# Performance work log

Hardware: AMD Instinct MI355X
Metric: run time of the kernel (lower is better)

The kernel has to match this reference:

```python
import jax, jax.numpy as jnp
import numpy as np

HEADS = 16
DIM_HEAD = 64
NPATCH = 256
LN_EPS = 1e-5


def setup_inputs() -> dict:
    key = jax.random.key(0)
    ks = jax.random.split(key, 6)
    B, S, D = 4, 2048, 1024
    inner = HEADS * DIM_HEAD  # 1024
    x = jax.random.normal(ks[0], (B, S, D), dtype=jnp.float32)
    ln_gamma = jnp.ones((D,), dtype=jnp.float32)
    ln_beta = jnp.zeros((D,), dtype=jnp.float32)
    # torch Linear: y = x @ W.T; we store the transposed weight directly.
    Wqkv = jax.random.normal(ks[1], (D, 3 * inner), dtype=jnp.float32) / np.sqrt(D)
    Wout = jax.random.normal(ks[2], (inner, D), dtype=jnp.float32) / np.sqrt(inner)
    bout = jnp.zeros((D,), dtype=jnp.float32)
    return {"x": x, "ln_gamma": ln_gamma, "ln_beta": ln_beta,
            "Wqkv": Wqkv, "Wout": Wout, "bout": bout}


def reference(x, ln_gamma, ln_beta, Wqkv, Wout, bout):
    B, S, D = x.shape
    # LayerNorm
    mu = jnp.mean(x, axis=-1, keepdims=True)
    var = jnp.mean(jnp.square(x - mu), axis=-1, keepdims=True)
    xn = (x - mu) * jax.lax.rsqrt(var + LN_EPS) * ln_gamma + ln_beta
    # QKV projection
    qkv = xn @ Wqkv  # [B, S, 3*H*Dh]
    q, k, v = jnp.split(qkv, 3, axis=-1)
    q = q.reshape(B, S, HEADS, DIM_HEAD)
    k = k.reshape(B, S, HEADS, DIM_HEAD)
    v = v.reshape(B, S, HEADS, DIM_HEAD)
    scale = DIM_HEAD ** -0.5
    dots = jnp.einsum('bqhd,bkhd->bhqk', q, k) * scale  # [B,H,S,S]
    # block-causal mask: query window i attends to key windows 0..i
    win = jnp.arange(S) // NPATCH
    mask = win[:, None] >= win[None, :]  # [S, S] bool
    dots = jnp.where(mask[None, None], dots, -jnp.inf)
    attn = jax.nn.softmax(dots, axis=-1)
    out = jnp.einsum('bhqk,bkhd->bqhd', attn, v).reshape(B, S, HEADS * DIM_HEAD)
    return out @ Wout + bout
```

## Files before the change

kernel.cpp:

```cpp
#include <hip/hip_runtime.h>
#include <stdint.h>

typedef unsigned short u16;
typedef __attribute__((ext_vector_type(8))) short bf16x8;
typedef __attribute__((ext_vector_type(4))) float f32x4;
typedef __attribute__((ext_vector_type(4))) unsigned short u16x4;
typedef __attribute__((ext_vector_type(4))) unsigned int u32x4;

#define DEVI static __device__ __forceinline__

#define QSCALE (0.125f * 1.4426950408889634f)

DEVI u16 f2bf(float f) {
  union { float f; unsigned int u; } v; v.f = f;
  unsigned int u = v.u + 0x7fffu + ((v.u >> 16) & 1u);
  return (u16)(u >> 16);
}
DEVI void gl16(const void* g, void* l) {
  __builtin_amdgcn_global_load_lds(
      (__attribute__((address_space(1))) void*)g,
      (__attribute__((address_space(3))) void*)l, 16, 0, 0);
}
DEVI unsigned int cvtpk(float a, float b) {
  unsigned int r;
  asm("v_cvt_pk_bf16_f32 %0, %1, %2" : "=v"(r) : "v"(a), "v"(b));
  return r;
}

__device__ const int QTMAP[16] = {15, 14, 13, 12, 8, 9, 10, 11,
                                  5, 4, 6, 7, 2, 3, 1, 0};

__global__ __launch_bounds__(256) void k_ln_split(
    const float* __restrict__ x, const float* __restrict__ gamma,
    const float* __restrict__ beta, u16* __restrict__ xh) {
  const int row = blockIdx.x;
  const int t = threadIdx.x;
  const float4* xr = (const float4*)(x + (size_t)row * 1024);
  float4 v = xr[t];
  float s = v.x + v.y + v.z + v.w;
  float s2 = v.x * v.x + v.y * v.y + v.z * v.z + v.w * v.w;
  #pragma unroll
  for (int m = 1; m < 64; m <<= 1) { s += __shfl_xor(s, m); s2 += __shfl_xor(s2, m); }
  __shared__ float ls[4], ls2[4];
  if ((t & 63) == 0) { ls[t >> 6] = s; ls2[t >> 6] = s2; }
  __syncthreads();
  s = ls[0] + ls[1] + ls[2] + ls[3];
  s2 = ls2[0] + ls2[1] + ls2[2] + ls2[3];
  float mu = s * (1.0f / 1024.0f);
  float var = s2 * (1.0f / 1024.0f) - mu * mu;
  float rstd = rsqrtf(var + 1e-5f);
  float4 g = ((const float4*)gamma)[t];
  float4 b = ((const float4*)beta)[t];
  float xv[4] = {v.x, v.y, v.z, v.w};
  float gg[4] = {g.x, g.y, g.z, g.w};
  float bb[4] = {b.x, b.y, b.z, b.w};
  u16x4 hv;
  #pragma unroll
  for (int i = 0; i < 4; i++) {
    float xn = (xv[i] - mu) * rstd * gg[i] + bb[i];
    hv[i] = f2bf(xn);
  }
  ((u16x4*)xh)[(size_t)row * 256 + t] = hv;
}

__global__ __launch_bounds__(256) void k_wsplit_t(
    const float* __restrict__ W, u16* __restrict__ Wth, int K, int N) {
  __shared__ float tile[32][33];
  const int t = threadIdx.x;
  const int tx = t & 31, ty = t >> 5;
  #pragma unroll
  for (int i = 0; i < 4; i++) {
    int k = blockIdx.y * 32 + ty + i * 8;
    int n = blockIdx.x * 32 + tx;
    tile[ty + i * 8][tx] = W[(size_t)k * N + n];
  }
  __syncthreads();
  #pragma unroll
  for (int i = 0; i < 4; i++) {
    int n = blockIdx.x * 32 + ty + i * 8;
    int k = blockIdx.y * 32 + tx;
    Wth[(size_t)n * K + k] = f2bf(tile[tx][ty + i * 8]);
  }
}

template <int MODE>
__global__ __launch_bounds__(256) void k_gemm(
    const u16* __restrict__ Ah, const u16* __restrict__ Bh,
    u16* __restrict__ Qh, u16* __restrict__ Kh, u16* __restrict__ Vth,
    float* __restrict__ Cout, const float* __restrict__ bias) {
  __shared__ u16 sAh[128 * 64];
  __shared__ u16 sBh[128 * 64];
  const int t = threadIdx.x, lane = t & 63, w = t >> 6;
  const int bm = blockIdx.x, bn = blockIdx.y;
  const int wm = (w >> 1) * 64, wn = (w & 1) * 64;
  const int g = lane >> 4, c = lane & 15;
  const size_t arow0 = (size_t)bm * 128, brow0 = (size_t)bn * 128;

  f32x4 acc[4][4] = {};

  for (int kt = 0; kt < 16; kt++) {
    __syncthreads();
    #pragma unroll
    for (int i = 0; i < 4; i++) {
      int ci = t + i * 256;
      int r = ci >> 3, cc = ci & 7;
      int cs = cc ^ (r & 7);
      size_t ka = (size_t)kt * 64 + cs * 8;
      gl16(Ah + (arow0 + r) * 1024 + ka, sAh + (size_t)ci * 8);
      gl16(Bh + (brow0 + r) * 1024 + ka, sBh + (size_t)ci * 8);
    }
    __syncthreads();
    #pragma unroll
    for (int ks = 0; ks < 2; ks++) {
      bf16x8 afh[4], bfh[4];
      #pragma unroll
      for (int mi = 0; mi < 4; mi++) {
        int row = wm + mi * 16 + c;
        afh[mi] = *(const bf16x8*)(sAh + row * 64 + (((ks * 4 + g) ^ (row & 7)) * 8));
      }
      #pragma unroll
      for (int ni = 0; ni < 4; ni++) {
        int row = wn + ni * 16 + c;
        bfh[ni] = *(const bf16x8*)(sBh + row * 64 + (((ks * 4 + g) ^ (row & 7)) * 8));
      }
      #pragma unroll
      for (int mi = 0; mi < 4; mi++)
        #pragma unroll
        for (int ni = 0; ni < 4; ni++)
          acc[mi][ni] = __builtin_amdgcn_mfma_f32_16x16x32_bf16(afh[mi], bfh[ni], acc[mi][ni], 0, 0, 0);
    }
  }

  if (MODE == 0) {
    #pragma unroll
    for (int mi = 0; mi < 4; mi++) {
      int grow0 = bm * 128 + wm + mi * 16 + g * 4;
      int b = grow0 >> 11, s0 = grow0 & 2047;
      #pragma unroll
      for (int ni = 0; ni < 4; ni++) {
        int gcol = bn * 128 + wn + ni * 16 + c;
        int which = gcol >> 10, rem = gcol & 1023;
        int hh = rem >> 6, dd = rem & 63;
        if (which == 2) {
          u16x4 hv;
          #pragma unroll
          for (int r = 0; r < 4; r++) hv[r] = f2bf(acc[mi][ni][r]);
          size_t off = ((size_t)((b * 16 + hh) * 64 + dd)) * 2048 + s0;
          *(u16x4*)(Vth + off) = hv;
        } else {
          u16* dh = which ? Kh : Qh;
          float sc = which ? 1.0f : QSCALE;
          #pragma unroll
          for (int r = 0; r < 4; r++) {
            size_t off = ((size_t)(b * 16 + hh) * 2048 + (s0 + r)) * 64 + dd;
            dh[off] = f2bf(acc[mi][ni][r] * sc);
          }
        }
      }
    }
  } else {
    #pragma unroll
    for (int mi = 0; mi < 4; mi++) {
      int grow0 = bm * 128 + wm + mi * 16 + g * 4;
      #pragma unroll
      for (int ni = 0; ni < 4; ni++) {
        int gcol = bn * 128 + wn + ni * 16 + c;
        float bb = bias[gcol];
        #pragma unroll
        for (int r = 0; r < 4; r++)
          Cout[(size_t)(grow0 + r) * 1024 + gcol] = acc[mi][ni][r] + bb;
      }
    }
  }
}

__global__ __launch_bounds__(512, 4) void k_attn(
    const u16* __restrict__ Qh, const u16* __restrict__ Kh,
    const u16* __restrict__ Vth, u16* __restrict__ Oh) {
  __shared__ u16 lK[2][64 * 64], lV[2][64 * 64];
  const int t = threadIdx.x, lane = t & 63, w = t >> 6;
  const int bh = blockIdx.x;
  const int qt = QTMAP[blockIdx.y];
  const int b = bh >> 4, h = bh & 15;
  const int qrow0 = qt * 128;
  const int kvlen = (qt / 2 + 1) * 256;
  const int g = lane >> 4, c = lane & 15;

  bf16x8 qf[2];
  {
    const u16* qb = Qh + ((size_t)bh * 2048 + qrow0 + w * 16) * 64;
    #pragma unroll
    for (int ks = 0; ks < 2; ks++)
      qf[ks] = *(const bf16x8*)(qb + (size_t)c * 64 + ks * 32 + g * 8);
  }

  const u16* Kb = Kh + (size_t)bh * 2048 * 64;
  const u16* Vb = Vth + (size_t)bh * 64 * 2048;

  const int ci = t;
  const int r0 = ci >> 3, cc0 = ci & 7;
  const int cs0 = cc0 ^ (r0 & 7);

  float mrun = -INFINITY, lrun = 0.f;
  f32x4 o[4] = {};

  const int ntiles = kvlen >> 6;

  gl16(Kb + (size_t)r0 * 64 + cs0 * 8, lK[0] + (size_t)ci * 8);
  gl16(Vb + (size_t)r0 * 2048 + cs0 * 8, lV[0] + (size_t)ci * 8);
  __syncthreads();

  const u16* gK = Kb + (size_t)(64 + r0) * 64 + cs0 * 8;
  const u16* gV = Vb + (size_t)r0 * 2048 + 64 + cs0 * 8;

  for (int kt = 0; kt < ntiles; kt++) {
    const int cur = kt & 1, nxt = cur ^ 1;
    if (kt + 1 < ntiles) {
      gl16(gK, lK[nxt] + (size_t)ci * 8);  gK += 64 * 64;
      gl16(gV, lV[nxt] + (size_t)ci * 8);  gV += 64;
    }

    f32x4 s[4] = {};
    __builtin_amdgcn_s_setprio(1);
    #pragma unroll
    for (int ni = 0; ni < 4; ni++) {
      int kr = ni * 16 + c;
      #pragma unroll
      for (int ks = 0; ks < 2; ks++) {
        int off = kr * 64 + ((ks * 4 + g) ^ (kr & 7)) * 8;
        bf16x8 kf = *(const bf16x8*)(lK[cur] + off);
        s[ni] = __builtin_amdgcn_mfma_f32_16x16x32_bf16(kf, qf[ks], s[ni], 0, 0, 0);
      }
    }
    __builtin_amdgcn_s_setprio(0);

    float a0 = fmaxf(fmaxf(s[0][0], s[0][1]), fmaxf(s[0][2], s[0][3]));
    float a1 = fmaxf(fmaxf(s[1][0], s[1][1]), fmaxf(s[1][2], s[1][3]));
    float a2 = fmaxf(fmaxf(s[2][0], s[2][1]), fmaxf(s[2][2], s[2][3]));
    float a3 = fmaxf(fmaxf(s[3][0], s[3][1]), fmaxf(s[3][2], s[3][3]));
    float tl = fmaxf(fmaxf(a0, a1), fmaxf(a2, a3));
    if (!__all(tl - mrun <= 8.0f)) {
      float tm = tl;
      tm = fmaxf(tm, __shfl_xor(tm, 16));
      tm = fmaxf(tm, __shfl_xor(tm, 32));
      float mnew = fmaxf(mrun, tm);
      float al = exp2f(mrun - mnew);
      mrun = mnew;
      lrun *= al;
      #pragma unroll
      for (int r = 0; r < 4; r++) {
        float ar = __shfl(al, g * 4 + r);
        #pragma unroll
        for (int di = 0; di < 4; di++) o[di][r] *= ar;
      }
    }

    #pragma unroll
    for (int ni = 0; ni < 4; ni++)
      #pragma unroll
      for (int r = 0; r < 4; r++)
        s[ni][r] = exp2f(s[ni][r] - mrun);
    #pragma unroll
    for (int ni = 0; ni < 4; ni++)
      lrun += (s[ni][0] + s[ni][1]) + (s[ni][2] + s[ni][3]);
    unsigned int Wd[4][2];
    #pragma unroll
    for (int ni = 0; ni < 4; ni++)
      #pragma unroll
      for (int rp = 0; rp < 2; rp++)
        Wd[ni][rp] = cvtpk(s[ni][2 * rp], s[ni][2 * rp + 1]);
    bf16x8 pa[2];
    #pragma unroll
    for (int ks = 0; ks < 2; ks++) {
      unsigned int e0 = Wd[2 * ks][0], f0 = Wd[2 * ks + 1][0];
      unsigned int e1 = Wd[2 * ks][1], f1 = Wd[2 * ks + 1][1];
      asm volatile("v_permlane32_swap_b32 %0, %1" : "+v"(e0), "+v"(f0));
      asm volatile("v_permlane16_swap_b32 %0, %1" : "+v"(e0), "+v"(f0));
      asm volatile("v_permlane32_swap_b32 %0, %1" : "+v"(e1), "+v"(f1));
      asm volatile("v_permlane16_swap_b32 %0, %1" : "+v"(e1), "+v"(f1));
      union { u32x4 u; bf16x8 bv; } cvu;
      cvu.u = (u32x4){e0, e1, f0, f1};
      pa[ks] = cvu.bv;
    }

    __builtin_amdgcn_s_setprio(1);
    #pragma unroll
    for (int di = 0; di < 4; di++) {
      int vr = di * 16 + c;
      #pragma unroll
      for (int ks = 0; ks < 2; ks++) {
        int off = vr * 64 + ((ks * 4 + g) ^ (vr & 7)) * 8;
        bf16x8 vf = *(const bf16x8*)(lV[cur] + off);
        o[di] = __builtin_amdgcn_mfma_f32_16x16x32_bf16(pa[ks], vf, o[di], 0, 0, 0);
      }
    }
    __builtin_amdgcn_s_setprio(0);

    __syncthreads();
  }

  float lf = lrun;
  lf += __shfl_xor(lf, 16);
  lf += __shfl_xor(lf, 32);
  float inv = 1.0f / lf;
  #pragma unroll
  for (int r = 0; r < 4; r++) {
    float ir = __shfl(inv, g * 4 + r);
    int srow = qrow0 + w * 16 + g * 4 + r;
    size_t rowo = ((size_t)b * 2048 + srow) * 1024 + h * 64;
    #pragma unroll
    for (int di = 0; di < 4; di++)
      Oh[rowo + di * 16 + c] = f2bf(o[di][r] * ir);
  }
}

extern "C" void kernel_launch(void* const* d_in, const int* in_sizes, int n_in,
                              void* d_out, int out_size, void* d_ws, size_t ws_size,
                              hipStream_t stream) {
  const float* x     = (const float*)d_in[0];
  const float* gamma = (const float*)d_in[1];
  const float* beta  = (const float*)d_in[2];
  const float* Wqkv  = (const float*)d_in[3];
  const float* Wout  = (const float*)d_in[4];
  const float* bout  = (const float*)d_in[5];
  float* out = (float*)d_out;

  char* ws = (char*)d_ws;
  size_t off = 0;
  auto alloc = [&](size_t bytes) { char* p = ws + off; off += (bytes + 255) & ~(size_t)255; return p; };
  const size_t SZ_XN = (size_t)8192 * 1024 * 2;
  const size_t SZ_WQ = (size_t)3072 * 1024 * 2;
  const size_t SZ_WO = (size_t)1024 * 1024 * 2;
  const size_t SZ_QKV = (size_t)4 * 16 * 2048 * 64 * 2;
  u16* xnh  = (u16*)alloc(SZ_XN);
  u16* wqth = (u16*)alloc(SZ_WQ);
  u16* woth = (u16*)alloc(SZ_WO);
  u16* Qh  = (u16*)alloc(SZ_QKV);
  u16* Kh  = (u16*)alloc(SZ_QKV);
  u16* Vth = (u16*)alloc(SZ_QKV);
  if (off > ws_size) return;

  k_ln_split<<<8192, 256, 0, stream>>>(x, gamma, beta, xnh);
  k_wsplit_t<<<dim3(96, 32), 256, 0, stream>>>(Wqkv, wqth, 1024, 3072);
  k_wsplit_t<<<dim3(32, 32), 256, 0, stream>>>(Wout, woth, 1024, 1024);
  k_gemm<0><<<dim3(64, 24), 256, 0, stream>>>(xnh, wqth,
                                              Qh, Kh, Vth, nullptr, nullptr);
  k_attn<<<dim3(64, 16), 512, 0, stream>>>(Qh, Kh, Vth, xnh);
  k_gemm<1><<<dim3(64, 8), 256, 0, stream>>>(xnh, woth,
                                             nullptr, nullptr, nullptr,
                                             out, bout);
}
```

Before: 180.2 us.

## Pair heavy and light query tiles per attention block and swizzle GEMM tile order

The attention kernel now runs two query tiles per block, pairing tile 15-y with tile y, so every block does an equal amount of block-causal work and the grid is halved; this replaces the static QTMAP ordering. LDS read offsets for the K/V fragments are precomputed once per thread, and the row-max reduction is regrouped. The GEMM kernels remap block indices with an 8-way XCD-style swizzle so that neighbouring tiles share L2. The halved attention grid reduces parallelism (512 blocks), and the second tile reloads K/V from scratch.

```diff
diff --git a/kernel.cpp b/kernel.cpp
--- a/kernel.cpp
+++ b/kernel.cpp
@@ -26,9 +26,6 @@
   asm("v_cvt_pk_bf16_f32 %0, %1, %2" : "=v"(r) : "v"(a), "v"(b));
   return r;
 }
-
-__device__ const int QTMAP[16] = {15, 14, 13, 12, 8, 9, 10, 11,
-                                  5, 4, 6, 7, 2, 3, 1, 0};
 
 __global__ __launch_bounds__(256) void k_ln_split(
     const float* __restrict__ x, const float* __restrict__ gamma,
@@ -91,7 +88,10 @@
   __shared__ u16 sAh[128 * 64];
   __shared__ u16 sBh[128 * 64];
   const int t = threadIdx.x, lane = t & 63, w = t >> 6;
-  const int bm = blockIdx.x, bn = blockIdx.y;
+  const int flat = blockIdx.y * gridDim.x + blockIdx.x;
+  const int per = (gridDim.x * gridDim.y) >> 3;
+  const int swz = (flat & 7) * per + (flat >> 3);
+  const int bm = swz & 63, bn = swz >> 6;
   const int wm = (w >> 1) * 64, wn = (w & 1) * 64;
   const int g = lane >> 4, c = lane & 15;
   const size_t arow0 = (size_t)bm * 128, brow0 = (size_t)bn * 128;
@@ -180,137 +180,143 @@
   __shared__ u16 lK[2][64 * 64], lV[2][64 * 64];
   const int t = threadIdx.x, lane = t & 63, w = t >> 6;
   const int bh = blockIdx.x;
-  const int qt = QTMAP[blockIdx.y];
   const int b = bh >> 4, h = bh & 15;
-  const int qrow0 = qt * 128;
-  const int kvlen = (qt / 2 + 1) * 256;
   const int g = lane >> 4, c = lane & 15;
-
-  bf16x8 qf[2];
-  {
-    const u16* qb = Qh + ((size_t)bh * 2048 + qrow0 + w * 16) * 64;
-    #pragma unroll
-    for (int ks = 0; ks < 2; ks++)
-      qf[ks] = *(const bf16x8*)(qb + (size_t)c * 64 + ks * 32 + g * 8);
-  }
 
   const u16* Kb = Kh + (size_t)bh * 2048 * 64;
   const u16* Vb = Vth + (size_t)bh * 64 * 2048;
+
+  int roff[4][2];
+  #pragma unroll
+  for (int i = 0; i < 4; i++)
+    #pragma unroll
+    for (int ks = 0; ks < 2; ks++) {
+      int row = i * 16 + c;
+      roff[i][ks] = row * 64 + (((ks * 4 + g) ^ (row & 7)) * 8);
+    }
 
   const int ci = t;
   const int r0 = ci >> 3, cc0 = ci & 7;
   const int cs0 = cc0 ^ (r0 & 7);
 
-  float mrun = -INFINITY, lrun = 0.f;
-  f32x4 o[4] = {};
-
-  const int ntiles = kvlen >> 6;
-
-  gl16(Kb + (size_t)r0 * 64 + cs0 * 8, lK[0] + (size_t)ci * 8);
-  gl16(Vb + (size_t)r0 * 2048 + cs0 * 8, lV[0] + (size_t)ci * 8);
-  __syncthreads();
-
-  const u16* gK = Kb + (size_t)(64 + r0) * 64 + cs0 * 8;
-  const u16* gV = Vb + (size_t)r0 * 2048 + 64 + cs0 * 8;
-
-  for (int kt = 0; kt < ntiles; kt++) {
-    const int cur = kt & 1, nxt = cur ^ 1;
-    if (kt + 1 < ntiles) {
-      gl16(gK, lK[nxt] + (size_t)ci * 8);  gK += 64 * 64;
-      gl16(gV, lV[nxt] + (size_t)ci * 8);  gV += 64;
-    }
-
-    f32x4 s[4] = {};
-    __builtin_amdgcn_s_setprio(1);
-    #pragma unroll
-    for (int ni = 0; ni < 4; ni++) {
-      int kr = ni * 16 + c;
+  for (int half = 0; half < 2; half++) {
+    const int qt = half ? blockIdx.y : 15 - blockIdx.y;
+    const int qrow0 = qt * 128;
+    const int ntiles = ((qt >> 1) + 1) * 4;
+
+    bf16x8 qf[2];
+    {
+      const u16* qb = Qh + ((size_t)bh * 2048 + qrow0 + w * 16) * 64;
+      #pragma unroll
+      for (int ks = 0; ks < 2; ks++)
+        qf[ks] = *(const bf16x8*)(qb + (size_t)c * 64 + ks * 32 + g * 8);
+    }
+
+    float mrun = -INFINITY, lrun = 0.f;
+    f32x4 o[4] = {};
+
+    gl16(Kb + (size_t)r0 * 64 + cs0 * 8, lK[0] + (size_t)ci * 8);
+    gl16(Vb + (size_t)r0 * 2048 + cs0 * 8, lV[0] + (size_t)ci * 8);
+    __syncthreads();
+
+    const u16* gK = Kb + (size_t)(64 + r0) * 64 + cs0 * 8;
+    const u16* gV = Vb + (size_t)r0 * 2048 + 64 + cs0 * 8;
+
+    for (int kt = 0; kt < ntiles; kt++) {
+      const int cur = kt & 1, nxt = cur ^ 1;
+      if (kt + 1 < ntiles) {
+        gl16(gK, lK[nxt] + (size_t)ci * 8);  gK += 64 * 64;
+        gl16(gV, lV[nxt] + (size_t)ci * 8);  gV += 64;
+      }
+
+      f32x4 s[4] = {};
+      __builtin_amdgcn_s_setprio(1);
+      #pragma unroll
+      for (int ni = 0; ni < 4; ni++)
+        #pragma unroll
+        for (int ks = 0; ks < 2; ks++) {
+          bf16x8 kf = *(const bf16x8*)(lK[cur] + roff[ni][ks]);
+          s[ni] = __builtin_amdgcn_mfma_f32_16x16x32_bf16(kf, qf[ks], s[ni], 0, 0, 0);
+        }
+      __builtin_amdgcn_s_setprio(0);
+
+      float A0 = fmaxf(fmaxf(s[0][0], s[0][1]), s[0][2]);
+      float A1 = fmaxf(fmaxf(s[0][3], s[1][0]), s[1][1]);
+      float A2 = fmaxf(fmaxf(s[1][2], s[1][3]), s[2][0]);
+      float A3 = fmaxf(fmaxf(s[2][1], s[2][2]), s[2][3]);
+      float A4 = fmaxf(fmaxf(s[3][0], s[3][1]), s[3][2]);
+      float B0 = fmaxf(fmaxf(A0, A1), A2);
+      float tl = fmaxf(fmaxf(fmaxf(B0, A3), A4), s[3][3]);
+      if (!__all(tl - mrun <= 8.0f)) {
+        float tm = tl;
+        tm = fmaxf(tm, __shfl_xor(tm, 16));
+        tm = fmaxf(tm, __shfl_xor(tm, 32));
+        float mnew = fmaxf(mrun, tm);
+        float al = exp2f(mrun - mnew);
+        mrun = mnew;
+        lrun *= al;
+        #pragma unroll
+        for (int r = 0; r < 4; r++) {
+          float ar = __shfl(al, g * 4 + r);
+          #pragma unroll
+          for (int di = 0; di < 4; di++) o[di][r] *= ar;
+        }
+      }
+
+      #pragma unroll
+      for (int ni = 0; ni < 4; ni++)
+        #pragma unroll
+        for (int r = 0; r < 4; r++)
+          s[ni][r] = exp2f(s[ni][r] - mrun);
+      #pragma unroll
+      for (int ni = 0; ni < 4; ni++)
+        lrun += (s[ni][0] + s[ni][1]) + (s[ni][2] + s[ni][3]);
+      unsigned int Wd[4][2];
+      #pragma unroll
+      for (int ni = 0; ni < 4; ni++)
+        #pragma unroll
+        for (int rp = 0; rp < 2; rp++)
+          Wd[ni][rp] = cvtpk(s[ni][2 * rp], s[ni][2 * rp + 1]);
+      bf16x8 pa[2];
       #pragma unroll
       for (int ks = 0; ks < 2; ks++) {
-        int off = kr * 64 + ((ks * 4 + g) ^ (kr & 7)) * 8;
-        bf16x8 kf = *(const bf16x8*)(lK[cur] + off);
-        s[ni] = __builtin_amdgcn_mfma_f32_16x16x32_bf16(kf, qf[ks], s[ni], 0, 0, 0);
-      }
-    }
-    __builtin_amdgcn_s_setprio(0);
-
-    float a0 = fmaxf(fmaxf(s[0][0], s[0][1]), fmaxf(s[0][2], s[0][3]));
-    float a1 = fmaxf(fmaxf(s[1][0], s[1][1]), fmaxf(s[1][2], s[1][3]));
-    float a2 = fmaxf(fmaxf(s[2][0], s[2][1]), fmaxf(s[2][2], s[2][3]));
-    float a3 = fmaxf(fmaxf(s[3][0], s[3][1]), fmaxf(s[3][2], s[3][3]));
-    float tl = fmaxf(fmaxf(a0, a1), fmaxf(a2, a3));
-    if (!__all(tl - mrun <= 8.0f)) {
-      float tm = tl;
-      tm = fmaxf(tm, __shfl_xor(tm, 16));
-      tm = fmaxf(tm, __shfl_xor(tm, 32));
-      float mnew = fmaxf(mrun, tm);
-      float al = exp2f(mrun - mnew);
-      mrun = mnew;
-      lrun *= al;
-      #pragma unroll
-      for (int r = 0; r < 4; r++) {
-        float ar = __shfl(al, g * 4 + r);
-        #pragma unroll
-        for (int di = 0; di < 4; di++) o[di][r] *= ar;
-      }
-    }
-
-    #pragma unroll
-    for (int ni = 0; ni < 4; ni++)
-      #pragma unroll
-      for (int r = 0; r < 4; r++)
-        s[ni][r] = exp2f(s[ni][r] - mrun);
-    #pragma unroll
-    for (int ni = 0; ni < 4; ni++)
-      lrun += (s[ni][0] + s[ni][1]) + (s[ni][2] + s[ni][3]);
-    unsigned int Wd[4][2];
-    #pragma unroll
-    for (int ni = 0; ni < 4; ni++)
-      #pragma unroll
-      for (int rp = 0; rp < 2; rp++)
-        Wd[ni][rp] = cvtpk(s[ni][2 * rp], s[ni][2 * rp + 1]);
-    bf16x8 pa[2];
-    #pragma unroll
-    for (int ks = 0; ks < 2; ks++) {
-      unsigned int e0 = Wd[2 * ks][0], f0 = Wd[2 * ks + 1][0];
-      unsigned int e1 = Wd[2 * ks][1], f1 = Wd[2 * ks + 1][1];
-      asm volatile("v_permlane32_swap_b32 %0, %1" : "+v"(e0), "+v"(f0));
-      asm volatile("v_permlane16_swap_b32 %0, %1" : "+v"(e0), "+v"(f0));
-      asm volatile("v_permlane32_swap_b32 %0, %1" : "+v"(e1), "+v"(f1));
-      asm volatile("v_permlane16_swap_b32 %0, %1" : "+v"(e1), "+v"(f1));
-      union { u32x4 u; bf16x8 bv; } cvu;
-      cvu.u = (u32x4){e0, e1, f0, f1};
-      pa[ks] = cvu.bv;
-    }
-
-    __builtin_amdgcn_s_setprio(1);
-    #pragma unroll
-    for (int di = 0; di < 4; di++) {
-      int vr = di * 16 + c;
-      #pragma unroll
-      for (int ks = 0; ks < 2; ks++) {
-        int off = vr * 64 + ((ks * 4 + g) ^ (vr & 7)) * 8;
-        bf16x8 vf = *(const bf16x8*)(lV[cur] + off);
-        o[di] = __builtin_amdgcn_mfma_f32_16x16x32_bf16(pa[ks], vf, o[di], 0, 0, 0);
-      }
-    }
-    __builtin_amdgcn_s_setprio(0);
-
-    __syncthreads();
-  }
-
-  float lf = lrun;
-  lf += __shfl_xor(lf, 16);
-  lf += __shfl_xor(lf, 32);
-  float inv = 1.0f / lf;
-  #pragma unroll
-  for (int r = 0; r < 4; r++) {
-    float ir = __shfl(inv, g * 4 + r);
-    int srow = qrow0 + w * 16 + g * 4 + r;
-    size_t rowo = ((size_t)b * 2048 + srow) * 1024 + h * 64;
-    #pragma unroll
-    for (int di = 0; di < 4; di++)
-      Oh[rowo + di * 16 + c] = f2bf(o[di][r] * ir);
+        unsigned int e0 = Wd[2 * ks][0], f0 = Wd[2 * ks + 1][0];
+        unsigned int e1 = Wd[2 * ks][1], f1 = Wd[2 * ks + 1][1];
+        asm volatile("v_permlane32_swap_b32 %0, %1" : "+v"(e0), "+v"(f0));
+        asm volatile("v_permlane16_swap_b32 %0, %1" : "+v"(e0), "+v"(f0));
+        asm volatile("v_permlane32_swap_b32 %0, %1" : "+v"(e1), "+v"(f1));
+        asm volatile("v_permlane16_swap_b32 %0, %1" : "+v"(e1), "+v"(f1));
+        union { u32x4 u; bf16x8 bv; } cvu;
+        cvu.u = (u32x4){e0, e1, f0, f1};
+        pa[ks] = cvu.bv;
+      }
+
+      __builtin_amdgcn_s_setprio(1);
+      #pragma unroll
+      for (int di = 0; di < 4; di++)
+        #pragma unroll
+        for (int ks = 0; ks < 2; ks++) {
+          bf16x8 vf = *(const bf16x8*)(lV[cur] + roff[di][ks]);
+          o[di] = __builtin_amdgcn_mfma_f32_16x16x32_bf16(pa[ks], vf, o[di], 0, 0, 0);
+        }
+      __builtin_amdgcn_s_setprio(0);
+
+      __syncthreads();
+    }
+
+    float lf = lrun;
+    lf += __shfl_xor(lf, 16);
+    lf += __shfl_xor(lf, 32);
+    float inv = 1.0f / lf;
+    #pragma unroll
+    for (int r = 0; r < 4; r++) {
+      float ir = __shfl(inv, g * 4 + r);
+      int srow = qrow0 + w * 16 + g * 4 + r;
+      size_t rowo = ((size_t)b * 2048 + srow) * 1024 + h * 64;
+      #pragma unroll
+      for (int di = 0; di < 4; di++)
+        Oh[rowo + di * 16 + c] = f2bf(o[di][r] * ir);
+    }
   }
 }
 
@@ -345,7 +351,7 @@
   k_wsplit_t<<<dim3(32, 32), 256, 0, stream>>>(Wout, woth, 1024, 1024);
   k_gemm<0><<<dim3(64, 24), 256, 0, stream>>>(xnh, wqth,
                                               Qh, Kh, Vth, nullptr, nullptr);
-  k_attn<<<dim3(64, 16), 512, 0, stream>>>(Qh, Kh, Vth, xnh);
+  k_attn<<<dim3(64, 8), 512, 0, stream>>>(Qh, Kh, Vth, xnh);
   k_gemm<1><<<dim3(64, 8), 256, 0, stream>>>(xnh, woth,
                                              nullptr, nullptr, nullptr,
                                              out, bout);
```

Result: slower. 196.3 us (+9.0%).

## Widen attention KV tile to 128, fold max into MFMA init, MFMA row-sum

Applied to the files above, without the earlier changes.

The attention kernel now processes 128 keys per iteration instead of 64, doubling the LDS tiles and halving the loop count and barriers. The running max is subtracted by initializing the score accumulators to -mrun, so the separate subtraction pass goes away, and exp2 uses raw v_exp_f32 inline asm. Row sums are now computed with an extra MFMA against a ones vector instead of scalar adds plus shuffles. The q-tile order mapping is simplified to a plain reverse order. In exchange there is more LDS and register pressure at 4 blocks per CU, the rows are summed from bf16-rounded probabilities, and the max/rescale logic now starts from a zero baseline.

```diff
diff --git a/kernel.cpp b/kernel.cpp
--- a/kernel.cpp
+++ b/kernel.cpp
@@ -26,9 +26,14 @@
   asm("v_cvt_pk_bf16_f32 %0, %1, %2" : "=v"(r) : "v"(a), "v"(b));
   return r;
 }
-
-__device__ const int QTMAP[16] = {15, 14, 13, 12, 8, 9, 10, 11,
-                                  5, 4, 6, 7, 2, 3, 1, 0};
+DEVI float fexp2(float x) {
+  float r;
+  asm("v_exp_f32 %0, %1\n\ts_nop 0" : "=v"(r) : "v"(x));
+  return r;
+}
+DEVI float fmax4(f32x4 v) {
+  return fmaxf(fmaxf(v[0], v[1]), fmaxf(v[2], v[3]));
+}
 
 __global__ __launch_bounds__(256) void k_ln_split(
     const float* __restrict__ x, const float* __restrict__ gamma,
@@ -177,10 +182,10 @@
 __global__ __launch_bounds__(512, 4) void k_attn(
     const u16* __restrict__ Qh, const u16* __restrict__ Kh,
     const u16* __restrict__ Vth, u16* __restrict__ Oh) {
-  __shared__ u16 lK[2][64 * 64], lV[2][64 * 64];
+  __shared__ u16 lK[2][128 * 64], lV[2][64 * 128];
   const int t = threadIdx.x, lane = t & 63, w = t >> 6;
   const int bh = blockIdx.x;
-  const int qt = QTMAP[blockIdx.y];
+  const int qt = 15 - blockIdx.y;
   const int b = bh >> 4, h = bh & 15;
   const int qrow0 = qt * 128;
   const int kvlen = (qt / 2 + 1) * 256;
@@ -197,83 +202,85 @@
   const u16* Kb = Kh + (size_t)bh * 2048 * 64;
   const u16* Vb = Vth + (size_t)bh * 64 * 2048;
 
-  const int ci = t;
-  const int r0 = ci >> 3, cc0 = ci & 7;
-  const int cs0 = cc0 ^ (r0 & 7);
-
-  float mrun = -INFINITY, lrun = 0.f;
+  int kbase[2], vbase[4];
+  #pragma unroll
+  for (int ks = 0; ks < 2; ks++) kbase[ks] = c * 64 + (((ks * 4 + g) ^ (c & 7)) * 8);
+  #pragma unroll
+  for (int ks = 0; ks < 4; ks++) vbase[ks] = c * 128 + (((ks * 4 + g) ^ c) * 8);
+
+  const int kr0 = t >> 3, kcs0 = (t & 7) ^ (kr0 & 7);
+  const int vr0 = t >> 4, vcs0 = (t & 15) ^ (vr0 & 15);
+
+  const bf16x8 vones = {(short)0x3F80, (short)0x3F80, (short)0x3F80, (short)0x3F80,
+                        (short)0x3F80, (short)0x3F80, (short)0x3F80, (short)0x3F80};
+
+  float mrun = 0.f;
+  f32x4 lsum = {0.f, 0.f, 0.f, 0.f};
   f32x4 o[4] = {};
 
-  const int ntiles = kvlen >> 6;
-
-  gl16(Kb + (size_t)r0 * 64 + cs0 * 8, lK[0] + (size_t)ci * 8);
-  gl16(Vb + (size_t)r0 * 2048 + cs0 * 8, lV[0] + (size_t)ci * 8);
+  const int ntiles = kvlen >> 7;
+
+  gl16(Kb + (size_t)kr0 * 64 + kcs0 * 8, lK[0] + (size_t)t * 8);
+  gl16(Kb + (size_t)(kr0 + 64) * 64 + kcs0 * 8, lK[0] + (size_t)(t + 512) * 8);
+  gl16(Vb + (size_t)vr0 * 2048 + vcs0 * 8, lV[0] + (size_t)t * 8);
+  gl16(Vb + (size_t)(vr0 + 32) * 2048 + vcs0 * 8, lV[0] + (size_t)(t + 512) * 8);
   __syncthreads();
 
-  const u16* gK = Kb + (size_t)(64 + r0) * 64 + cs0 * 8;
-  const u16* gV = Vb + (size_t)r0 * 2048 + 64 + cs0 * 8;
+  const u16* gK = Kb + (size_t)(128 + kr0) * 64 + kcs0 * 8;
+  const u16* gV = Vb + (size_t)vr0 * 2048 + 128 + vcs0 * 8;
 
   for (int kt = 0; kt < ntiles; kt++) {
     const int cur = kt & 1, nxt = cur ^ 1;
     if (kt + 1 < ntiles) {
-      gl16(gK, lK[nxt] + (size_t)ci * 8);  gK += 64 * 64;
-      gl16(gV, lV[nxt] + (size_t)ci * 8);  gV += 64;
-    }
-
-    f32x4 s[4] = {};
+      gl16(gK, lK[nxt] + (size_t)t * 8);
+      gl16(gK + 64 * 64, lK[nxt] + (size_t)(t + 512) * 8);
+      gl16(gV, lV[nxt] + (size_t)t * 8);
+      gl16(gV + 32 * 2048, lV[nxt] + (size_t)(t + 512) * 8);
+      gK += 128 * 64;  gV += 128;
+    }
+
+    f32x4 s[8];
+    #pragma unroll
+    for (int ni = 0; ni < 8; ni++)
+      s[ni] = (f32x4){-mrun, -mrun, -mrun, -mrun};
     __builtin_amdgcn_s_setprio(1);
     #pragma unroll
-    for (int ni = 0; ni < 4; ni++) {
-      int kr = ni * 16 + c;
+    for (int ni = 0; ni < 8; ni++)
       #pragma unroll
       for (int ks = 0; ks < 2; ks++) {
-        int off = kr * 64 + ((ks * 4 + g) ^ (kr & 7)) * 8;
-        bf16x8 kf = *(const bf16x8*)(lK[cur] + off);
+        bf16x8 kf = *(const bf16x8*)(lK[cur] + ni * 1024 + kbase[ks]);
         s[ni] = __builtin_amdgcn_mfma_f32_16x16x32_bf16(kf, qf[ks], s[ni], 0, 0, 0);
       }
-    }
     __builtin_amdgcn_s_setprio(0);
 
-    float a0 = fmaxf(fmaxf(s[0][0], s[0][1]), fmaxf(s[0][2], s[0][3]));
-    float a1 = fmaxf(fmaxf(s[1][0], s[1][1]), fmaxf(s[1][2], s[1][3]));
-    float a2 = fmaxf(fmaxf(s[2][0], s[2][1]), fmaxf(s[2][2], s[2][3]));
-    float a3 = fmaxf(fmaxf(s[3][0], s[3][1]), fmaxf(s[3][2], s[3][3]));
-    float tl = fmaxf(fmaxf(a0, a1), fmaxf(a2, a3));
-    if (!__all(tl - mrun <= 8.0f)) {
-      float tm = tl;
-      tm = fmaxf(tm, __shfl_xor(tm, 16));
+    float tl = fmaxf(fmaxf(fmaxf(fmax4(s[0]), fmax4(s[1])), fmaxf(fmax4(s[2]), fmax4(s[3]))),
+                     fmaxf(fmaxf(fmax4(s[4]), fmax4(s[5])), fmaxf(fmax4(s[6]), fmax4(s[7]))));
+    if (!__all(tl <= 8.0f)) {
+      float tm = fmaxf(tl, __shfl_xor(tl, 16));
       tm = fmaxf(tm, __shfl_xor(tm, 32));
-      float mnew = fmaxf(mrun, tm);
-      float al = exp2f(mrun - mnew);
-      mrun = mnew;
-      lrun *= al;
+      float delta = fmaxf(tm, 0.0f);
+      mrun += delta;
+      float al = fexp2(-delta);
+      #pragma unroll
+      for (int ni = 0; ni < 8; ni++)
+        #pragma unroll
+        for (int r = 0; r < 4; r++) s[ni][r] -= delta;
       #pragma unroll
       for (int r = 0; r < 4; r++) {
         float ar = __shfl(al, g * 4 + r);
+        lsum[r] *= ar;
         #pragma unroll
         for (int di = 0; di < 4; di++) o[di][r] *= ar;
       }
     }
 
-    #pragma unroll
-    for (int ni = 0; ni < 4; ni++)
-      #pragma unroll
-      for (int r = 0; r < 4; r++)
-        s[ni][r] = exp2f(s[ni][r] - mrun);
-    #pragma unroll
-    for (int ni = 0; ni < 4; ni++)
-      lrun += (s[ni][0] + s[ni][1]) + (s[ni][2] + s[ni][3]);
-    unsigned int Wd[4][2];
-    #pragma unroll
-    for (int ni = 0; ni < 4; ni++)
-      #pragma unroll
-      for (int rp = 0; rp < 2; rp++)
-        Wd[ni][rp] = cvtpk(s[ni][2 * rp], s[ni][2 * rp + 1]);
-    bf16x8 pa[2];
-    #pragma unroll
-    for (int ks = 0; ks < 2; ks++) {
-      unsigned int e0 = Wd[2 * ks][0], f0 = Wd[2 * ks + 1][0];
-      unsigned int e1 = Wd[2 * ks][1], f1 = Wd[2 * ks + 1][1];
+    bf16x8 pa[4];
+    #pragma unroll
+    for (int ks = 0; ks < 4; ks++) {
+      unsigned int e0 = cvtpk(fexp2(s[2 * ks][0]), fexp2(s[2 * ks][1]));
+      unsigned int e1 = cvtpk(fexp2(s[2 * ks][2]), fexp2(s[2 * ks][3]));
+      unsigned int f0 = cvtpk(fexp2(s[2 * ks + 1][0]), fexp2(s[2 * ks + 1][1]));
+      unsigned int f1 = cvtpk(fexp2(s[2 * ks + 1][2]), fexp2(s[2 * ks + 1][3]));
       asm volatile("v_permlane32_swap_b32 %0, %1" : "+v"(e0), "+v"(f0));
       asm volatile("v_permlane16_swap_b32 %0, %1" : "+v"(e0), "+v"(f0));
       asm volatile("v_permlane32_swap_b32 %0, %1" : "+v"(e1), "+v"(f1));
@@ -285,27 +292,23 @@
 
     __builtin_amdgcn_s_setprio(1);
     #pragma unroll
-    for (int di = 0; di < 4; di++) {
-      int vr = di * 16 + c;
-      #pragma unroll
-      for (int ks = 0; ks < 2; ks++) {
-        int off = vr * 64 + ((ks * 4 + g) ^ (vr & 7)) * 8;
-        bf16x8 vf = *(const bf16x8*)(lV[cur] + off);
+    for (int di = 0; di < 4; di++)
+      #pragma unroll
+      for (int ks = 0; ks < 4; ks++) {
+        bf16x8 vf = *(const bf16x8*)(lV[cur] + di * 2048 + vbase[ks]);
         o[di] = __builtin_amdgcn_mfma_f32_16x16x32_bf16(pa[ks], vf, o[di], 0, 0, 0);
       }
-    }
+    #pragma unroll
+    for (int ks = 0; ks < 4; ks++)
+      lsum = __builtin_amdgcn_mfma_f32_16x16x32_bf16(pa[ks], vones, lsum, 0, 0, 0);
     __builtin_amdgcn_s_setprio(0);
 
     __syncthreads();
   }
 
-  float lf = lrun;
-  lf += __shfl_xor(lf, 16);
-  lf += __shfl_xor(lf, 32);
-  float inv = 1.0f / lf;
   #pragma unroll
   for (int r = 0; r < 4; r++) {
-    float ir = __shfl(inv, g * 4 + r);
+    float ir = 1.0f / lsum[r];
     int srow = qrow0 + w * 16 + g * 4 + r;
     size_t rowo = ((size_t)b * 2048 + srow) * 1024 + h * 64;
     #pragma unroll
```

Result: faster. 163.9 us (-9.0%).
